# Kernel tuning notes

Measured on AMD Instinct MI355X. Metric: run time of the kernel, lower is better.

Reference implementation:

```python
import jax, jax.numpy as jnp
import numpy as np

D = 384
EPS = 1e-12  # F.normalize eps


def setup_inputs() -> dict:
    key = jax.random.key(0)
    ks = jax.random.split(key, 12)
    s = 1.0 / np.sqrt(D)  # torch Linear default init scale
    return {
        "x": jax.random.normal(ks[0], (8192, D), jnp.float32),
        "y": jax.random.normal(ks[1], (8192, D), jnp.float32),
        "Wq": jax.random.uniform(ks[2], (D, D), jnp.float32, -s, s),
        "bq": jax.random.uniform(ks[3], (D,), jnp.float32, -s, s),
        "Wk": jax.random.uniform(ks[4], (D, D), jnp.float32, -s, s),
        "bk": jax.random.uniform(ks[5], (D,), jnp.float32, -s, s),
        "Wv": jax.random.uniform(ks[6], (D, D), jnp.float32, -s, s),
        "bv": jax.random.uniform(ks[7], (D,), jnp.float32, -s, s),
        "Wo": jax.random.uniform(ks[8], (D, D), jnp.float32, -s, s),
        "bo": jax.random.uniform(ks[9], (D,), jnp.float32, -s, s),
    }


def reference(x, y, Wq, bq, Wk, bk, Wv, bv, Wo, bo):
    # Q: [N, d], K/V: [M, d]
    Q = x @ Wq.T + bq
    K = y @ Wk.T + bk
    V = y @ Wv.T + bv
    scale = 1.0 / jnp.sqrt(jnp.asarray(Q.shape[-1], Q.dtype))
    attn = jax.nn.softmax((Q @ K.T) * scale, axis=-1)  # [N, M]
    ctx = attn @ V  # [N, d]
    # F.normalize(p=2, dim=1): divide by max(||row||_2, eps)
    norm = jnp.maximum(jnp.linalg.norm(ctx, axis=1, keepdims=True), EPS)
    ctx = ctx / norm
    return (x + ctx) @ Wo.T + bo
```

## Files before the change

kernel.cpp:

```cpp
#include <hip/hip_runtime.h>
#include <stdint.h>


typedef __attribute__((ext_vector_type(8))) short bf16x8;
typedef __attribute__((ext_vector_type(4))) float f32x4;

#define DEV static __device__ __forceinline__

DEV short f2bf(float f) {
  uint32_t u = __builtin_bit_cast(uint32_t, f);
  u += 0x7fffu + ((u >> 16) & 1u);
  return (short)(u >> 16);
}
DEV uint32_t pack2(float a, float b) {
  return (uint32_t)(uint16_t)f2bf(a) | ((uint32_t)(uint16_t)f2bf(b) << 16);
}

template <int BIAS_ON_N, int OUT_F32, int A_F32>
__global__ __launch_bounds__(256) void gemm_nt(
    const void* __restrict__ Aptr, const float* __restrict__ B,
    const float* __restrict__ bias, void* __restrict__ Cptr,
    int M, int N, int K) {
  __shared__ char As[128 * 128];
  __shared__ char Bs[128 * 128];
  const int tid = threadIdx.x;
  const int l = tid & 63, w = tid >> 6;
  const int lq = l & 15, lk = l >> 4;
  const int m0 = blockIdx.x * 128, n0 = blockIdx.y * 128;
  const int wr = (w >> 1) * 64, wc = (w & 1) * 64;
  f32x4 acc[4][4] = {};

  for (int k0 = 0; k0 < K; k0 += 64) {
    if (A_F32) {
      const float* A = (const float*)Aptr;
#pragma unroll
      for (int i = 0; i < 8; i++) {
        int c = tid + i * 256;
        int row = c >> 4, col = (c & 15) * 4;
        f32x4 v = *(const f32x4*)(A + (size_t)(m0 + row) * K + k0 + col);
        uint32_t lo = pack2(v.x, v.y), hi = pack2(v.z, v.w);
        int off = (row * 128 + col * 2) ^ ((row & 7) << 4);
        *(uint32_t*)(As + off) = lo;
        *(uint32_t*)(As + off + 4) = hi;
      }
    } else {
      const short* A = (const short*)Aptr;
#pragma unroll
      for (int i = 0; i < 4; i++) {
        int c = tid + i * 256;
        int row = c >> 3, col = (c & 7) * 8;
        uint4 v = *(const uint4*)(A + (size_t)(m0 + row) * K + k0 + col);
        int off = (row * 128 + col * 2) ^ ((row & 7) << 4);
        *(uint4*)(As + off) = v;
      }
    }
#pragma unroll
    for (int i = 0; i < 8; i++) {
      int c = tid + i * 256;
      int row = c >> 4, col = (c & 15) * 4;
      f32x4 v = *(const f32x4*)(B + (size_t)(n0 + row) * K + k0 + col);
      uint32_t lo = pack2(v.x, v.y), hi = pack2(v.z, v.w);
      int off = (row * 128 + col * 2) ^ ((row & 7) << 4);
      *(uint32_t*)(Bs + off) = lo;
      *(uint32_t*)(Bs + off + 4) = hi;
    }
    __syncthreads();
#pragma unroll
    for (int ks = 0; ks < 2; ks++) {
      bf16x8 af[4], bfr[4];
#pragma unroll
      for (int m = 0; m < 4; m++) {
        int row = wr + m * 16 + lq;
        af[m] = *(const bf16x8*)(As + ((row * 128 + ks * 64 + lk * 16) ^ ((row & 7) << 4)));
      }
#pragma unroll
      for (int n = 0; n < 4; n++) {
        int row = wc + n * 16 + lq;
        bfr[n] = *(const bf16x8*)(Bs + ((row * 128 + ks * 64 + lk * 16) ^ ((row & 7) << 4)));
      }
#pragma unroll
      for (int m = 0; m < 4; m++)
#pragma unroll
        for (int n = 0; n < 4; n++)
          acc[m][n] = __builtin_amdgcn_mfma_f32_16x16x32_bf16(af[m], bfr[n], acc[m][n], 0, 0, 0);
    }
    __syncthreads();
  }
#pragma unroll
  for (int m = 0; m < 4; m++) {
    int mg = m0 + wr + m * 16 + lk * 4;
#pragma unroll
    for (int n = 0; n < 4; n++) {
      int ng = n0 + wc + n * 16 + lq;
#pragma unroll
      for (int r = 0; r < 4; r++) {
        float v = acc[m][n][r] + (BIAS_ON_N ? bias[ng] : bias[mg + r]);
        if (OUT_F32)
          ((float*)Cptr)[(size_t)(mg + r) * N + ng] = v;
        else
          ((short*)Cptr)[(size_t)(mg + r) * N + ng] = f2bf(v);
      }
    }
  }
}

#define FSPLIT 4
#define KVB 32
#define KVRANGE 2048

__global__ __launch_bounds__(256, 2) void flash_attn(
    const short* __restrict__ Qb, const short* __restrict__ Kb,
    const short* __restrict__ Vt, float* __restrict__ ctx_part) {
  __shared__ char Ks[32 * 768];
  __shared__ char Vs[384 * 80];
  __shared__ char Ps[64 * 80];
  const int tid = threadIdx.x, l = tid & 63, w = tid >> 6;
  const int lq = l & 15, lk = l >> 4;
  const int sp = blockIdx.x & 3, qt = blockIdx.x >> 2;
  const int q0 = qt * 64 + w * 16;
  const float sc = 0.05103103630798288f * 1.4426950408889634f;

  bf16x8 qf[12];
#pragma unroll
  for (int ks = 0; ks < 12; ks++)
    qf[ks] = *(const bf16x8*)(Qb + (size_t)(q0 + lq) * 384 + ks * 32 + lk * 8);

  f32x4 acc[24] = {};

  for (int t = 0; t < KVRANGE / KVB; t++) {
    const int kv0 = sp * KVRANGE + t * KVB;
#pragma unroll
    for (int i = 0; i < 6; i++) {
      int c = tid + i * 256;
      int row = c / 48, cb = (c % 48) * 16;
      uint4 v = *(const uint4*)((const char*)Kb + (size_t)(kv0 + row) * 768 + cb);
      *(uint4*)(Ks + ((row * 768 + cb) ^ ((row & 7) << 4))) = v;
    }
#pragma unroll
    for (int i = 0; i < 6; i++) {
      int c = tid + i * 256;
      int d = c >> 2, part = c & 3;
      uint4 v = *(const uint4*)((const char*)Vt + (size_t)d * 16384 + (size_t)(kv0 + part * 8) * 2);
      *(uint4*)(Vs + d * 80 + part * 16) = v;
    }
    __syncthreads();

    f32x4 s0a = {}, s0b = {}, s1a = {}, s1b = {};
#pragma unroll
    for (int ks = 0; ks < 12; ks += 2) {
      int colb = ks * 64 + lk * 16;
      int r0 = lq, r1 = 16 + lq;
      bf16x8 b0 = *(const bf16x8*)(Ks + ((r0 * 768 + colb) ^ ((r0 & 7) << 4)));
      bf16x8 b1 = *(const bf16x8*)(Ks + ((r1 * 768 + colb) ^ ((r1 & 7) << 4)));
      bf16x8 b2 = *(const bf16x8*)(Ks + ((r0 * 768 + colb + 64) ^ ((r0 & 7) << 4)));
      bf16x8 b3 = *(const bf16x8*)(Ks + ((r1 * 768 + colb + 64) ^ ((r1 & 7) << 4)));
      s0a = __builtin_amdgcn_mfma_f32_16x16x32_bf16(qf[ks], b0, s0a, 0, 0, 0);
      s1a = __builtin_amdgcn_mfma_f32_16x16x32_bf16(qf[ks], b1, s1a, 0, 0, 0);
      s0b = __builtin_amdgcn_mfma_f32_16x16x32_bf16(qf[ks + 1], b2, s0b, 0, 0, 0);
      s1b = __builtin_amdgcn_mfma_f32_16x16x32_bf16(qf[ks + 1], b3, s1b, 0, 0, 0);
    }
#pragma unroll
    for (int r = 0; r < 4; r++) {
      int prow = w * 16 + lk * 4 + r;
      float p0 = exp2f((s0a[r] + s0b[r]) * sc);
      float p1 = exp2f((s1a[r] + s1b[r]) * sc);
      *(short*)(Ps + prow * 80 + lq * 2) = f2bf(p0);
      *(short*)(Ps + prow * 80 + 32 + lq * 2) = f2bf(p1);
    }
    asm volatile("s_waitcnt lgkmcnt(0)" ::: "memory");
    bf16x8 pa = *(const bf16x8*)(Ps + (w * 16 + lq) * 80 + lk * 16);
#pragma unroll
    for (int nf = 0; nf < 24; nf++) {
      bf16x8 bv = *(const bf16x8*)(Vs + (nf * 16 + lq) * 80 + lk * 16);
      acc[nf] = __builtin_amdgcn_mfma_f32_16x16x32_bf16(pa, bv, acc[nf], 0, 0, 0);
    }
    __syncthreads();
  }
  float* out = ctx_part + (size_t)sp * 8192 * 384;
#pragma unroll
  for (int nf = 0; nf < 24; nf++) {
    int d = nf * 16 + lq;
#pragma unroll
    for (int r = 0; r < 4; r++) {
      int q = q0 + lk * 4 + r;
      out[(size_t)q * 384 + d] = acc[nf][r];
    }
  }
}

__global__ __launch_bounds__(256) void combine_norm(
    const float* __restrict__ ctx_part, const float* __restrict__ x,
    short* __restrict__ Xn) {
  const int l = threadIdx.x & 63, w = threadIdx.x >> 6;
  const int q = blockIdx.x * 4 + w;
  const size_t SLAB = (size_t)8192 * 384;
  float v[6];
  float ss = 0.f;
#pragma unroll
  for (int i = 0; i < 6; i++) {
    size_t off = (size_t)q * 384 + i * 64 + l;
    float s = ctx_part[off] + ctx_part[off + SLAB] + ctx_part[off + 2 * SLAB] +
              ctx_part[off + 3 * SLAB];
    v[i] = s;
    ss += s * s;
  }
#pragma unroll
  for (int m = 1; m <= 32; m <<= 1) ss += __shfl_xor(ss, m);
  float inv = 1.0f / fmaxf(sqrtf(ss), 1e-12f);
#pragma unroll
  for (int i = 0; i < 6; i++) {
    size_t off = (size_t)q * 384 + i * 64 + l;
    Xn[off] = f2bf(x[off] + v[i] * inv);
  }
}

extern "C" void kernel_launch(void* const* d_in, const int* in_sizes, int n_in,
                              void* d_out, int out_size, void* d_ws, size_t ws_size,
                              hipStream_t stream) {
  (void)in_sizes; (void)n_in; (void)out_size; (void)ws_size;
  const float* x  = (const float*)d_in[0];
  const float* y  = (const float*)d_in[1];
  const float* Wq = (const float*)d_in[2];
  const float* bq = (const float*)d_in[3];
  const float* Wk = (const float*)d_in[4];
  const float* bk = (const float*)d_in[5];
  const float* Wv = (const float*)d_in[6];
  const float* bv = (const float*)d_in[7];
  const float* Wo = (const float*)d_in[8];
  const float* bo = (const float*)d_in[9];

  char* ws = (char*)d_ws;
  short* Qb = (short*)(ws);
  short* Kb = (short*)(ws + 6291456);
  short* Vt = (short*)(ws + 12582912);
  short* Xn = (short*)(ws + 18874368);
  float* ctx = (float*)(ws + 25165824);

  dim3 blk(256);
  gemm_nt<1, 0, 1><<<dim3(64, 3), blk, 0, stream>>>(x, Wq, bq, Qb, 8192, 384, 384);
  gemm_nt<1, 0, 1><<<dim3(64, 3), blk, 0, stream>>>(y, Wk, bk, Kb, 8192, 384, 384);
  gemm_nt<0, 0, 1><<<dim3(3, 64), blk, 0, stream>>>(Wv, y, bv, Vt, 384, 8192, 384);
  flash_attn<<<dim3(512), blk, 0, stream>>>(Qb, Kb, Vt, ctx);
  combine_norm<<<dim3(2048), blk, 0, stream>>>(ctx, x, Xn);
  gemm_nt<1, 1, 0><<<dim3(64, 3), blk, 0, stream>>>(Xn, Wo, bo, (float*)d_out, 8192, 384, 384);
}
```

Before: 318.1 us.

## Rewrite flash attention with 32x32 MFMA, async LDS loads and K double-buffering

Restructures the attention kernel around 32x32x16 bf16 MFMAs. Each wave now computes a 32-query tile, with waves split across halves of the head dimension. K and V are loaded asynchronously into LDS via global_load_lds, and K is double-buffered so the next tile's load overlaps the current compute. P stays in registers using cvt_pk and permlane32_swap instead of a round trip through shared memory, and the softmax scale with log2e is folded into the Q projection epilogue. In exchange it adds more register pressure (24 Q fragments) and hand-placed waitcnt/barrier logic that must be correct.

```diff
diff --git a/kernel.cpp b/kernel.cpp
--- a/kernel.cpp
+++ b/kernel.cpp
@@ -4,6 +4,7 @@
 
 typedef __attribute__((ext_vector_type(8))) short bf16x8;
 typedef __attribute__((ext_vector_type(4))) float f32x4;
+typedef __attribute__((ext_vector_type(16))) float f32x16;
 
 #define DEV static __device__ __forceinline__
 
@@ -15,12 +16,25 @@
 DEV uint32_t pack2(float a, float b) {
   return (uint32_t)(uint16_t)f2bf(a) | ((uint32_t)(uint16_t)f2bf(b) << 16);
 }
+DEV unsigned cvt_pk(float lo, float hi) {
+  unsigned r;
+  asm("v_cvt_pk_bf16_f32 %0, %1, %2" : "=v"(r) : "v"(lo), "v"(hi));
+  return r;
+}
+DEV void pl32swap(unsigned& a, unsigned& b) {
+  asm volatile("v_permlane32_swap_b32 %0, %1" : "+v"(a), "+v"(b));
+}
+DEV void gload16(const void* g, void* l) {
+  __builtin_amdgcn_global_load_lds(
+      (const __attribute__((address_space(1))) unsigned*)g,
+      (__attribute__((address_space(3))) unsigned*)l, 16, 0, 0);
+}
 
 template <int BIAS_ON_N, int OUT_F32, int A_F32>
 __global__ __launch_bounds__(256) void gemm_nt(
     const void* __restrict__ Aptr, const float* __restrict__ B,
     const float* __restrict__ bias, void* __restrict__ Cptr,
-    int M, int N, int K) {
+    int M, int N, int K, float scale) {
   __shared__ char As[128 * 128];
   __shared__ char Bs[128 * 128];
   const int tid = threadIdx.x;
@@ -94,7 +108,7 @@
       int ng = n0 + wc + n * 16 + lq;
 #pragma unroll
       for (int r = 0; r < 4; r++) {
-        float v = acc[m][n][r] + (BIAS_ON_N ? bias[ng] : bias[mg + r]);
+        float v = (acc[m][n][r] + (BIAS_ON_N ? bias[ng] : bias[mg + r])) * scale;
         if (OUT_F32)
           ((float*)Cptr)[(size_t)(mg + r) * N + ng] = v;
         else
@@ -104,86 +118,124 @@
   }
 }
 
-#define FSPLIT 4
-#define KVB 32
-#define KVRANGE 2048
+#define ITERS 64
 
 __global__ __launch_bounds__(256, 2) void flash_attn(
     const short* __restrict__ Qb, const short* __restrict__ Kb,
     const short* __restrict__ Vt, float* __restrict__ ctx_part) {
-  __shared__ char Ks[32 * 768];
-  __shared__ char Vs[384 * 80];
-  __shared__ char Ps[64 * 80];
+  __shared__ char Ks[2][24576];
+  __shared__ char Vs[24576];
   const int tid = threadIdx.x, l = tid & 63, w = tid >> 6;
-  const int lq = l & 15, lk = l >> 4;
+  const int l31 = l & 31, h = l >> 5;
+  const int qh = w >> 1, dh = w & 1;
   const int sp = blockIdx.x & 3, qt = blockIdx.x >> 2;
-  const int q0 = qt * 64 + w * 16;
-  const float sc = 0.05103103630798288f * 1.4426950408889634f;
-
-  bf16x8 qf[12];
-#pragma unroll
-  for (int ks = 0; ks < 12; ks++)
-    qf[ks] = *(const bf16x8*)(Qb + (size_t)(q0 + lq) * 384 + ks * 32 + lk * 8);
-
-  f32x4 acc[24] = {};
-
-  for (int t = 0; t < KVRANGE / KVB; t++) {
-    const int kv0 = sp * KVRANGE + t * KVB;
+  const int q0 = qt * 64 + qh * 32;
+  const int kvbase = sp * 2048;
+
+  bf16x8 qf[24];
+  {
+    const short* qrow = Qb + (size_t)(q0 + l31) * 384 + h * 8;
+#pragma unroll
+    for (int s = 0; s < 24; s++) qf[s] = *(const bf16x8*)(qrow + s * 16);
+  }
+  asm volatile("s_waitcnt vmcnt(0)" ::: "memory");
+
+  {
 #pragma unroll
     for (int i = 0; i < 6; i++) {
-      int c = tid + i * 256;
-      int row = c / 48, cb = (c % 48) * 16;
-      uint4 v = *(const uint4*)((const char*)Kb + (size_t)(kv0 + row) * 768 + cb);
-      *(uint4*)(Ks + ((row * 768 + cb) ^ ((row & 7) << 4))) = v;
-    }
-#pragma unroll
-    for (int i = 0; i < 6; i++) {
-      int c = tid + i * 256;
-      int d = c >> 2, part = c & 3;
-      uint4 v = *(const uint4*)((const char*)Vt + (size_t)d * 16384 + (size_t)(kv0 + part * 8) * 2);
-      *(uint4*)(Vs + d * 80 + part * 16) = v;
-    }
-    __syncthreads();
-
-    f32x4 s0a = {}, s0b = {}, s1a = {}, s1b = {};
-#pragma unroll
-    for (int ks = 0; ks < 12; ks += 2) {
-      int colb = ks * 64 + lk * 16;
-      int r0 = lq, r1 = 16 + lq;
-      bf16x8 b0 = *(const bf16x8*)(Ks + ((r0 * 768 + colb) ^ ((r0 & 7) << 4)));
-      bf16x8 b1 = *(const bf16x8*)(Ks + ((r1 * 768 + colb) ^ ((r1 & 7) << 4)));
-      bf16x8 b2 = *(const bf16x8*)(Ks + ((r0 * 768 + colb + 64) ^ ((r0 & 7) << 4)));
-      bf16x8 b3 = *(const bf16x8*)(Ks + ((r1 * 768 + colb + 64) ^ ((r1 & 7) << 4)));
-      s0a = __builtin_amdgcn_mfma_f32_16x16x32_bf16(qf[ks], b0, s0a, 0, 0, 0);
-      s1a = __builtin_amdgcn_mfma_f32_16x16x32_bf16(qf[ks], b1, s1a, 0, 0, 0);
-      s0b = __builtin_amdgcn_mfma_f32_16x16x32_bf16(qf[ks + 1], b2, s0b, 0, 0, 0);
-      s1b = __builtin_amdgcn_mfma_f32_16x16x32_bf16(qf[ks + 1], b3, s1b, 0, 0, 0);
-    }
-#pragma unroll
-    for (int r = 0; r < 4; r++) {
-      int prow = w * 16 + lk * 4 + r;
-      float p0 = exp2f((s0a[r] + s0b[r]) * sc);
-      float p1 = exp2f((s1a[r] + s1b[r]) * sc);
-      *(short*)(Ps + prow * 80 + lq * 2) = f2bf(p0);
-      *(short*)(Ps + prow * 80 + 32 + lq * 2) = f2bf(p1);
-    }
-    asm volatile("s_waitcnt lgkmcnt(0)" ::: "memory");
-    bf16x8 pa = *(const bf16x8*)(Ps + (w * 16 + lq) * 80 + lk * 16);
-#pragma unroll
-    for (int nf = 0; nf < 24; nf++) {
-      bf16x8 bv = *(const bf16x8*)(Vs + (nf * 16 + lq) * 80 + lk * 16);
-      acc[nf] = __builtin_amdgcn_mfma_f32_16x16x32_bf16(pa, bv, acc[nf], 0, 0, 0);
-    }
-    __syncthreads();
-  }
-  float* out = ctx_part + (size_t)sp * 8192 * 384;
-#pragma unroll
-  for (int nf = 0; nf < 24; nf++) {
-    int d = nf * 16 + lq;
-#pragma unroll
-    for (int r = 0; r < 4; r++) {
-      int q = q0 + lk * 4 + r;
-      out[(size_t)q * 384 + d] = acc[nf][r];
+      int d = (w * 6 + i) * 1024 + l * 16;
+      int row = d / 768, c = d - row * 768;
+      int csrc = c ^ ((row & 7) << 4);
+      gload16((const char*)Kb + (size_t)(kvbase + row) * 768 + csrc,
+              (char*)Ks[0] + (w * 6 + i) * 1024);
+    }
+  }
+
+  f32x16 acc[6] = {};
+
+#pragma unroll 1
+  for (int t = 0; t < ITERS; t++) {
+    const char* Kc = Ks[t & 1];
+    {
+      int kv0 = kvbase + t * 32;
+#pragma unroll
+      for (int i = 0; i < 6; i++) {
+        int d = (w * 6 + i) * 1024 + l * 16;
+        int vrow = d >> 6, c = d & 63;
+        int csrc = c ^ (((vrow >> 1) & 3) << 4);
+        gload16((const char*)Vt + (size_t)vrow * 16384 + kv0 * 2 + csrc,
+                Vs + (w * 6 + i) * 1024);
+      }
+    }
+    asm volatile("s_waitcnt vmcnt(6)" ::: "memory");
+    __builtin_amdgcn_s_barrier();
+
+    f32x16 S0 = {}, S1 = {};
+    const int swzk = (l31 & 7) << 4;
+    __builtin_amdgcn_s_setprio(1);
+#pragma unroll
+    for (int s = 0; s < 24; s += 2) {
+      bf16x8 k0 = *(const bf16x8*)(Kc + l31 * 768 + ((s * 32 + h * 16) ^ swzk));
+      bf16x8 k1 = *(const bf16x8*)(Kc + l31 * 768 + (((s + 1) * 32 + h * 16) ^ swzk));
+      S0 = __builtin_amdgcn_mfma_f32_32x32x16_bf16(k0, qf[s], S0, 0, 0, 0);
+      S1 = __builtin_amdgcn_mfma_f32_32x32x16_bf16(k1, qf[s + 1], S1, 0, 0, 0);
+    }
+    __builtin_amdgcn_s_setprio(0);
+
+    if (t < ITERS - 1) {
+      int kv0 = kvbase + (t + 1) * 32;
+      char* Kn = (char*)Ks[(t & 1) ^ 1];
+#pragma unroll
+      for (int i = 0; i < 6; i++) {
+        int d = (w * 6 + i) * 1024 + l * 16;
+        int row = d / 768, c = d - row * 768;
+        int csrc = c ^ ((row & 7) << 4);
+        gload16((const char*)Kb + (size_t)(kv0 + row) * 768 + csrc, Kn + (w * 6 + i) * 1024);
+      }
+    }
+
+    float p[16];
+#pragma unroll
+    for (int i = 0; i < 16; i++) p[i] = __builtin_amdgcn_exp2f(S0[i] + S1[i]);
+    unsigned a0 = cvt_pk(p[0], p[1]), a1 = cvt_pk(p[2], p[3]);
+    unsigned a2 = cvt_pk(p[4], p[5]), a3 = cvt_pk(p[6], p[7]);
+    pl32swap(a0, a2); pl32swap(a1, a3);
+    uint4 pw0 = {a0, a1, a2, a3};
+    bf16x8 pf0 = __builtin_bit_cast(bf16x8, pw0);
+    unsigned b0 = cvt_pk(p[8], p[9]), b1 = cvt_pk(p[10], p[11]);
+    unsigned b2 = cvt_pk(p[12], p[13]), b3 = cvt_pk(p[14], p[15]);
+    pl32swap(b0, b2); pl32swap(b1, b3);
+    uint4 pw1 = {b0, b1, b2, b3};
+    bf16x8 pf1 = __builtin_bit_cast(bf16x8, pw1);
+
+    if (t < ITERS - 1)
+      asm volatile("s_waitcnt vmcnt(6)" ::: "memory");
+    else
+      asm volatile("s_waitcnt vmcnt(0)" ::: "memory");
+    __builtin_amdgcn_s_barrier();
+
+    __builtin_amdgcn_s_setprio(1);
+#pragma unroll
+    for (int nf = 0; nf < 6; nf++) {
+      int vr = dh * 192 + nf * 32 + l31;
+      int swz = ((vr >> 1) & 3) << 4;
+      bf16x8 v0 = *(const bf16x8*)(Vs + vr * 64 + ((h * 16) ^ swz));
+      bf16x8 v1 = *(const bf16x8*)(Vs + vr * 64 + ((32 + h * 16) ^ swz));
+      acc[nf] = __builtin_amdgcn_mfma_f32_32x32x16_bf16(v0, pf0, acc[nf], 0, 0, 0);
+      acc[nf] = __builtin_amdgcn_mfma_f32_32x32x16_bf16(v1, pf1, acc[nf], 0, 0, 0);
+    }
+    __builtin_amdgcn_s_setprio(0);
+    __builtin_amdgcn_s_barrier();
+  }
+
+  float* outp = ctx_part + (size_t)sp * 8192 * 384 + (size_t)(q0 + l31) * 384;
+#pragma unroll
+  for (int nf = 0; nf < 6; nf++) {
+#pragma unroll
+    for (int qd = 0; qd < 4; qd++) {
+      f32x4 v = {acc[nf][qd * 4 + 0], acc[nf][qd * 4 + 1],
+                 acc[nf][qd * 4 + 2], acc[nf][qd * 4 + 3]};
+      *(f32x4*)(outp + dh * 192 + nf * 32 + qd * 8 + h * 4) = v;
     }
   }
 }
@@ -236,11 +288,12 @@
   short* Xn = (short*)(ws + 18874368);
   float* ctx = (float*)(ws + 25165824);
 
+  const float SC = 0.07362233f;
   dim3 blk(256);
-  gemm_nt<1, 0, 1><<<dim3(64, 3), blk, 0, stream>>>(x, Wq, bq, Qb, 8192, 384, 384);
-  gemm_nt<1, 0, 1><<<dim3(64, 3), blk, 0, stream>>>(y, Wk, bk, Kb, 8192, 384, 384);
-  gemm_nt<0, 0, 1><<<dim3(3, 64), blk, 0, stream>>>(Wv, y, bv, Vt, 384, 8192, 384);
+  gemm_nt<1, 0, 1><<<dim3(64, 3), blk, 0, stream>>>(x, Wq, bq, Qb, 8192, 384, 384, SC);
+  gemm_nt<1, 0, 1><<<dim3(64, 3), blk, 0, stream>>>(y, Wk, bk, Kb, 8192, 384, 384, 1.0f);
+  gemm_nt<0, 0, 1><<<dim3(3, 64), blk, 0, stream>>>(Wv, y, bv, Vt, 384, 8192, 384, 1.0f);
   flash_attn<<<dim3(512), blk, 0, stream>>>(Qb, Kb, Vt, ctx);
   combine_norm<<<dim3(2048), blk, 0, stream>>>(ctx, x, Xn);
-  gemm_nt<1, 1, 0><<<dim3(64, 3), blk, 0, stream>>>(Xn, Wo, bo, (float*)d_out, 8192, 384, 384);
-}
+  gemm_nt<1, 1, 0><<<dim3(64, 3), blk, 0, stream>>>(Xn, Wo, bo, (float*)d_out, 8192, 384, 384, 1.0f);
+}
```

Measured after the change: 427.4 us. +34.4%, slower.
